# Performance work log

Hardware: AMD Instinct MI355X
Metric: run time of the kernel (lower is better)

Reference implementation:

```python
import jax, jax.numpy as jnp
import numpy as np

B, T, E, H = 4, 1024, 1024, 16
D = E // H  # head_size = 64
EPS = 1e-5


def layernorm(x, g, b):
    mu = jnp.mean(x, axis=-1, keepdims=True)
    var = jnp.mean(jnp.square(x - mu), axis=-1, keepdims=True)
    return (x - mu) * jax.lax.rsqrt(var + EPS) * g + b


def setup_inputs() -> dict:
    key = jax.random.key(0)
    ks = jax.random.split(key, 12)
    s = 0.02
    return {
        "x": jax.random.normal(ks[0], (B, T, E), dtype=jnp.float32),
        "ln1_g": jnp.ones((E,), jnp.float32),
        "ln1_b": jnp.zeros((E,), jnp.float32),
        "Wq": jax.random.normal(ks[1], (H, E, D), dtype=jnp.float32) * s,
        "Wk": jax.random.normal(ks[2], (H, E, D), dtype=jnp.float32) * s,
        "Wv": jax.random.normal(ks[3], (H, E, D), dtype=jnp.float32) * s,
        "Wp": jax.random.normal(ks[4], (E, E), dtype=jnp.float32) * s,
        "bp": jnp.zeros((E,), jnp.float32),
        "ln2_g": jnp.ones((E,), jnp.float32),
        "ln2_b": jnp.zeros((E,), jnp.float32),
        "W1": jax.random.normal(ks[5], (E, 4 * E), dtype=jnp.float32) * s,
        "b1": jnp.zeros((4 * E,), jnp.float32),
        "W2": jax.random.normal(ks[6], (4 * E, E), dtype=jnp.float32) * s,
        "b2": jnp.zeros((E,), jnp.float32),
    }


def reference(x, ln1_g, ln1_b, Wq, Wk, Wv, Wp, bp, ln2_g, ln2_b, W1, b1, W2, b2):
    # --- attention sub-block (pre-LN) ---
    h = layernorm(x, ln1_g, ln1_b)               # [B,T,E]
    q = jnp.einsum('bte,hed->bhtd', h, Wq)       # [B,H,T,D]
    k = jnp.einsum('bte,hed->bhtd', h, Wk)
    v = jnp.einsum('bte,hed->bhtd', h, Wv)
    # NOTE: original module has NO 1/sqrt(D) scaling and its 'tril' buffer is
    # all-ones, so masked_fill is a no-op -> full (non-causal) softmax.
    scores = jnp.einsum('bhtd,bhsd->bhts', q, k)  # [B,H,T,T]
    attn = jax.nn.softmax(scores, axis=-1)
    o = jnp.einsum('bhts,bhsd->bhtd', attn, v)    # [B,H,T,D]
    o = o.transpose(0, 2, 1, 3).reshape(x.shape[0], x.shape[1], -1)  # [B,T,E]
    x = x + o @ Wp + bp
    # --- feedforward sub-block (dropout is identity at eval) ---
    h2 = layernorm(x, ln2_g, ln2_b)
    x = x + jax.nn.relu(h2 @ W1 + b1) @ W2 + b2
    return x
```

## Files before the change

kernel.cpp:

```cpp
#include <hip/hip_runtime.h>
#include <hip/hip_bf16.h>

#define BB 4
#define TT 1024
#define EE 1024
#define HH 16
#define DD 64
#define MM 4096
#define NQKV 3072
#define E4 4096

using short8  = __attribute__((ext_vector_type(8))) short;
using short4v = __attribute__((ext_vector_type(4))) short;
using f32x4   = __attribute__((ext_vector_type(4))) float;

__device__ __forceinline__ short f2bf(float f) {
    __hip_bfloat16 h = __float2bfloat16(f);
    return *reinterpret_cast<short*>(&h);
}

__device__ __forceinline__ unsigned int cvtpk_bf16(float a, float b) {
    unsigned int w;
    asm("v_cvt_pk_bf16_f32 %0, %1, %2" : "=v"(w) : "v"(a), "v"(b));
    return w;
}

__device__ __forceinline__ void gld16(const void* g, void* l) {
    __builtin_amdgcn_global_load_lds((__attribute__((address_space(1))) void*)g,
                                     (__attribute__((address_space(3))) void*)l,
                                     16, 0, 0);
}

__global__ __launch_bounds__(256) void tcvt_kernel(const float* __restrict__ in,
                                                   short* __restrict__ out,
                                                   int R, int C) {
    __shared__ short tile[64][65];
    const int c0 = blockIdx.x * 64, r0 = blockIdx.y * 64;
    const int tr = threadIdx.x >> 6;
    const int tc = threadIdx.x & 63;
#pragma unroll
    for (int i = 0; i < 16; ++i) {
        int r = i * 4 + tr;
        tile[tc][r] = f2bf(in[(size_t)(r0 + r) * C + c0 + tc]);
    }
    __syncthreads();
#pragma unroll
    for (int i = 0; i < 16; ++i) {
        int c = i * 4 + tr;
        out[(size_t)(c0 + c) * R + r0 + tc] = tile[c][tc];
    }
}

__global__ __launch_bounds__(256) void pack_qkv_t(const float* __restrict__ Wq,
                                                  const float* __restrict__ Wk,
                                                  const float* __restrict__ Wv,
                                                  short* __restrict__ out) {
    __shared__ short tile[64][65];
    const int m = blockIdx.y;
    const int which = m >> 4, head = m & 15;
    const float* src = ((which == 0) ? Wq : (which == 1) ? Wk : Wv) + (size_t)head * EE * DD;
    const float scale = (which == 1) ? 1.44269504f : 1.0f;
    const int e0 = blockIdx.x * 64;
    const int tr = threadIdx.x >> 6, tc = threadIdx.x & 63;
#pragma unroll
    for (int i = 0; i < 16; ++i) {
        int e = i * 4 + tr;
        tile[tc][e] = f2bf(src[(size_t)(e0 + e) * DD + tc] * scale);
    }
    __syncthreads();
#pragma unroll
    for (int i = 0; i < 16; ++i) {
        int d = i * 4 + tr;
        out[(size_t)(which * 1024 + head * 64 + d) * EE + e0 + tc] = tile[d][tc];
    }
}

__global__ __launch_bounds__(256) void vtr_kernel(const short* __restrict__ qkv,
                                                  short* __restrict__ vT) {
    __shared__ short tile[64][68];
    const int b = blockIdx.z;
    const int t0 = blockIdx.x * 64, c0 = blockIdx.y * 64;
    const int tr = threadIdx.x >> 4;
    const int q4 = (threadIdx.x & 15) * 4;
#pragma unroll
    for (int i = 0; i < 4; ++i) {
        int t = i * 16 + tr;
        short4v v = *(const short4v*)&qkv[((size_t)b * TT + t0 + t) * NQKV + 2048 + c0 + q4];
        *(short4v*)&tile[t][q4] = v;
    }
    __syncthreads();
#pragma unroll
    for (int i = 0; i < 4; ++i) {
        int c = i * 16 + tr;
        short4v v;
        v[0] = tile[q4 + 0][c];
        v[1] = tile[q4 + 1][c];
        v[2] = tile[q4 + 2][c];
        v[3] = tile[q4 + 3][c];
        *(short4v*)&vT[((size_t)b * 1024 + c0 + c) * TT + t0 + q4] = v;
    }
}

__global__ __launch_bounds__(256) void ln_kernel(const float* __restrict__ x,
                                                 const float* __restrict__ g,
                                                 const float* __restrict__ b,
                                                 short* __restrict__ out) {
    __shared__ float red[4];
    const int row = blockIdx.x;
    const int tid = threadIdx.x;
    float4 v = *(const float4*)&x[(size_t)row * EE + tid * 4];
    float s = v.x + v.y + v.z + v.w;
#pragma unroll
    for (int off = 32; off >= 1; off >>= 1) s += __shfl_xor(s, off, 64);
    if ((tid & 63) == 0) red[tid >> 6] = s;
    __syncthreads();
    float mean = (red[0] + red[1] + red[2] + red[3]) * (1.0f / EE);
    __syncthreads();
    float d0 = v.x - mean, d1 = v.y - mean, d2 = v.z - mean, d3 = v.w - mean;
    s = d0 * d0 + d1 * d1 + d2 * d2 + d3 * d3;
#pragma unroll
    for (int off = 32; off >= 1; off >>= 1) s += __shfl_xor(s, off, 64);
    if ((tid & 63) == 0) red[tid >> 6] = s;
    __syncthreads();
    float var = (red[0] + red[1] + red[2] + red[3]) * (1.0f / EE);
    float rstd = rsqrtf(var + 1e-5f);
    int c = tid * 4;
    short4v o;
    o[0] = f2bf(d0 * rstd * g[c + 0] + b[c + 0]);
    o[1] = f2bf(d1 * rstd * g[c + 1] + b[c + 1]);
    o[2] = f2bf(d2 * rstd * g[c + 2] + b[c + 2]);
    o[3] = f2bf(d3 * rstd * g[c + 3] + b[c + 3]);
    *(short4v*)&out[(size_t)row * EE + c] = o;
}

template <bool HAS_BIAS, bool RELU>
__global__ __launch_bounds__(512, 2) void gemm256(const short* __restrict__ A,
                                                  const short* __restrict__ Bt,
                                                  const float* __restrict__ bias,
                                                  short* __restrict__ out,
                                                  int M, int N, int K) {
    __shared__ __align__(16) short Ab[2][2][8192];
    __shared__ __align__(16) short Bb[2][2][8192];

    const int tid = threadIdx.x;
    const int lane = tid & 63;
    const int wid = tid >> 6;
    const int wr = wid >> 2;
    const int wc = wid & 3;
    const int l15 = lane & 15, lhi = lane >> 4;
    const int rsw = l15 & 7;

    int wg = blockIdx.y * gridDim.x + blockIdx.x;
    const int chunk = (gridDim.x * gridDim.y) >> 3;
    wg = (wg & 7) * chunk + (wg >> 3);
    const int bx = wg % gridDim.x, by = wg / gridDim.x;
    const int row0 = by * 256, col0 = bx * 256;

    const int srow = tid >> 3;
    const int scol = (((tid & 7) ^ (srow & 7)) << 3);

    const int NT = K >> 6;

    f32x4 acc[8][4] = {};

    auto stageA = [&](int b, int h, int k0) {
#pragma unroll
        for (int j = 0; j < 2; ++j)
            gld16(&A[(size_t)(row0 + h * 128 + j * 64 + srow) * K + k0 + scol],
                  &Ab[b][h][j * 4096 + wid * 512]);
    };
    auto stageB = [&](int b, int h, int k0) {
#pragma unroll
        for (int j = 0; j < 2; ++j)
            gld16(&Bt[(size_t)(col0 + h * 128 + j * 64 + srow) * K + k0 + scol],
                  &Bb[b][h][j * 4096 + wid * 512]);
    };

    stageA(0, 0, 0); stageA(0, 1, 0);
    stageB(0, 0, 0); stageB(0, 1, 0);
    if (NT > 1) {
        stageB(1, 0, 64); stageB(1, 1, 64);
        asm volatile("s_waitcnt vmcnt(4)" ::: "memory");
    } else {
        asm volatile("s_waitcnt vmcnt(0)" ::: "memory");
    }
    __builtin_amdgcn_s_barrier();

    for (int u = 0; u < NT; ++u) {
        const int buf = u & 1;
        short8 bfr[4][2];
#pragma unroll
        for (int p = 0; p < 4; ++p) {
            if (p == 0) {
#pragma unroll
                for (int n = 0; n < 4; ++n)
#pragma unroll
                    for (int ks = 0; ks < 2; ++ks)
                        bfr[n][ks] = *(const short8*)&Bb[buf][wc >> 1]
                            [((wc & 1) * 64 + n * 16 + l15) * 64 +
                             (((ks << 2) + lhi) ^ rsw) * 8];
            }
            short8 af[2][2];
#pragma unroll
            for (int mi = 0; mi < 2; ++mi)
#pragma unroll
                for (int ks = 0; ks < 2; ++ks)
                    af[mi][ks] = *(const short8*)&Ab[buf][wr]
                        [((p * 2 + mi) * 16 + l15) * 64 +
                         (((ks << 2) + lhi) ^ rsw) * 8];
            if (p == 0 && u + 1 < NT) stageA(buf ^ 1, 0, (u + 1) << 6);
            if (p == 1 && u + 1 < NT) stageA(buf ^ 1, 1, (u + 1) << 6);
            if (p == 2 && u + 2 < NT) stageB(buf, 0, (u + 2) << 6);
            if (p == 3 && u + 2 < NT) stageB(buf, 1, (u + 2) << 6);
            __builtin_amdgcn_s_barrier();
            __builtin_amdgcn_s_setprio(1);
#pragma unroll
            for (int mi = 0; mi < 2; ++mi)
#pragma unroll
                for (int n = 0; n < 4; ++n)
#pragma unroll
                    for (int ks = 0; ks < 2; ++ks)
                        acc[p * 2 + mi][n] = __builtin_amdgcn_mfma_f32_16x16x32_bf16(
                            af[mi][ks], bfr[n][ks], acc[p * 2 + mi][n], 0, 0, 0);
            __builtin_amdgcn_s_setprio(0);
            if (p == 3 && u + 1 < NT) {
                if (u + 2 < NT) asm volatile("s_waitcnt vmcnt(4)" ::: "memory");
                else            asm volatile("s_waitcnt vmcnt(0)" ::: "memory");
            }
            __builtin_amdgcn_s_barrier();
        }
    }

#pragma unroll
    for (int m = 0; m < 8; ++m)
#pragma unroll
        for (int n = 0; n < 4; ++n)
#pragma unroll
            for (int r = 0; r < 4; ++r) {
                int row = row0 + wr * 128 + m * 16 + lhi * 4 + r;
                int col = col0 + wc * 64 + n * 16 + l15;
                float v = acc[m][n][r];
                if (HAS_BIAS) v += bias[col];
                if (RELU) v = fmaxf(v, 0.f);
                out[(size_t)row * N + col] = f2bf(v);
            }
}

template <int BN, int PIPE, bool HAS_BIAS, bool RELU, bool RESID, bool OUT_BF16>
__global__ __launch_bounds__(256) void gemm_bt(const short* __restrict__ A,
                                               const short* __restrict__ Bt,
                                               const float* __restrict__ bias,
                                               const float* __restrict__ resid,
                                               void* __restrict__ outp,
                                               int M, int N, int K) {
    constexpr int WRC = (BN == 128) ? 2 : 4;
    constexpr int WCC = (BN == 128) ? 2 : 1;
    constexpr int MI = 8 / WRC;
    constexpr int NI = BN / (16 * WCC);
    constexpr int BCH = BN / 32;
    constexpr int ASZ = 128 * 64, BSZ = BN * 64;

    __shared__ __align__(16) short As[(PIPE ? 2 : 1) * ASZ];
    __shared__ __align__(16) short Bs[(PIPE ? 2 : 1) * BSZ];

    const int tid = threadIdx.x;
    const int lane = tid & 63;
    const int wid = tid >> 6;
    const int wr = (WRC == 2) ? (wid >> 1) : wid;
    const int wc = (WCC == 2) ? (wid & 1) : 0;
    const int l15 = lane & 15, lhi = lane >> 4;

    int wg = blockIdx.y * gridDim.x + blockIdx.x;
    const int chunk = (gridDim.x * gridDim.y) >> 3;
    wg = (wg & 7) * chunk + (wg >> 3);
    const int bx = wg % gridDim.x;
    const int by = wg / gridDim.x;
    const int row0 = by * 128, col0 = bx * BN;

    const int srow = tid >> 3;
    const int scol = (((tid & 7) ^ (srow & 7)) << 3);
    const int rsw = l15 & 7;

    const int wrow0 = wr * (16 * MI);
    const int wcol0 = wc * (16 * NI);

    f32x4 acc[MI][NI] = {};

    auto stage = [&](int k0, int bs) {
#pragma unroll
        for (int ch = 0; ch < 4; ++ch)
            gld16(&A[(size_t)(row0 + ch * 32 + srow) * K + k0 + scol],
                  &As[bs * ASZ + ch * 2048 + wid * 512]);
#pragma unroll
        for (int ch = 0; ch < BCH; ++ch)
            gld16(&Bt[(size_t)(col0 + ch * 32 + srow) * K + k0 + scol],
                  &Bs[bs * BSZ + ch * 2048 + wid * 512]);
    };
    auto compute = [&](int bs) {
#pragma unroll
        for (int ks = 0; ks < 2; ++ks) {
            short8 af[MI], bf[NI];
#pragma unroll
            for (int mi = 0; mi < MI; ++mi)
                af[mi] = *(const short8*)&As[bs * ASZ + (wrow0 + mi * 16 + l15) * 64 +
                                             (((ks << 2) + lhi) ^ rsw) * 8];
#pragma unroll
            for (int ni = 0; ni < NI; ++ni)
                bf[ni] = *(const short8*)&Bs[bs * BSZ + (wcol0 + ni * 16 + l15) * 64 +
                                             (((ks << 2) + lhi) ^ rsw) * 8];
#pragma unroll
            for (int mi = 0; mi < MI; ++mi)
#pragma unroll
                for (int ni = 0; ni < NI; ++ni)
                    acc[mi][ni] = __builtin_amdgcn_mfma_f32_16x16x32_bf16(
                        af[mi], bf[ni], acc[mi][ni], 0, 0, 0);
        }
    };

    if (PIPE == 1) {
        const int nt = K >> 6;
        stage(0, 0);
        stage(64, 1);
        int cur = 0;
        for (int t = 0; t < nt; ++t) {
            if (t + 1 < nt) asm volatile("s_waitcnt vmcnt(6)" ::: "memory");
            else            asm volatile("s_waitcnt vmcnt(0)" ::: "memory");
            __builtin_amdgcn_s_barrier();
            __builtin_amdgcn_sched_barrier(0);
            compute(cur);
            __builtin_amdgcn_sched_barrier(0);
            __builtin_amdgcn_s_barrier();
            if (t + 2 < nt) stage((t + 2) << 6, cur);
            cur ^= 1;
        }
    } else {
        for (int k0 = 0; k0 < K; k0 += 64) {
            __syncthreads();
            stage(k0, 0);
            __syncthreads();
            compute(0);
        }
    }

    float* outf = (float*)outp;
    short* outb = (short*)outp;
#pragma unroll
    for (int mi = 0; mi < MI; ++mi)
#pragma unroll
        for (int ni = 0; ni < NI; ++ni)
#pragma unroll
            for (int r = 0; r < 4; ++r) {
                int row = row0 + wrow0 + mi * 16 + lhi * 4 + r;
                int col = col0 + wcol0 + ni * 16 + l15;
                float v = acc[mi][ni][r];
                if (HAS_BIAS) v += bias[col];
                if (RELU) v = fmaxf(v, 0.f);
                if (RESID) v += resid[(size_t)row * N + col];
                if (OUT_BF16) outb[(size_t)row * N + col] = f2bf(v);
                else outf[(size_t)row * N + col] = v;
            }
}

__global__ __launch_bounds__(256) void attn_kernel(const short* __restrict__ qkv,
                                                   const short* __restrict__ vT,
                                                   short* __restrict__ obuf) {
    __shared__ __align__(16) short Ks[2][64 * 64];
    __shared__ __align__(16) short Vs[2][64 * 64];
    __shared__ __align__(16) unsigned int Pl[4][2][16][40];
    const int tid = threadIdx.x;
    const int lane = tid & 63;
    const int wid = tid >> 6;
    const int l15 = lane & 15, lhi = lane >> 4;
    const int lhi4 = lhi * 4;

    const int nb = ((blockIdx.x & 7) << 6) + (blockIdx.x >> 3);
    const int b = nb >> 7;
    const int h = (nb >> 3) & 15;
    const int q0 = (nb & 7) << 7;
    const size_t rbase = (size_t)b * TT;
    const int hq = h * 64;
    const short* vg = vT + ((size_t)b * 1024 + hq) * TT;

    const int srow = tid >> 3;
    const int scol = (((tid & 7) ^ (srow & 7)) << 3);
    const int rsw = (l15 & 7);

    short8 aq[2][2];
#pragma unroll
    for (int g = 0; g < 2; ++g)
#pragma unroll
        for (int ks = 0; ks < 2; ++ks)
            aq[g][ks] = *(const short8*)&qkv[(rbase + q0 + wid * 32 + g * 16 + l15) * NQKV +
                                             hq + ks * 32 + lhi * 8];

    float mrun[2] = {-INFINITY, -INFINITY};
    float lsum[2] = {0.f, 0.f};
    f32x4 o[2][4] = {};

#pragma unroll
    for (int ch = 0; ch < 2; ++ch) {
        gld16(&qkv[(rbase + 0 + ch * 32 + srow) * NQKV + 1024 + hq + scol],
              &Ks[0][ch * 2048 + wid * 512]);
        gld16(&vg[(size_t)(ch * 32 + srow) * TT + 0 + scol],
              &Vs[0][ch * 2048 + wid * 512]);
    }
    __syncthreads();

    int cur = 0;
    for (int st = 0; st < TT; st += 64) {
        if (st + 64 < TT) {
#pragma unroll
            for (int ch = 0; ch < 2; ++ch) {
                gld16(&qkv[(rbase + st + 64 + ch * 32 + srow) * NQKV + 1024 + hq + scol],
                      &Ks[cur ^ 1][ch * 2048 + wid * 512]);
                gld16(&vg[(size_t)(ch * 32 + srow) * TT + st + 64 + scol],
                      &Vs[cur ^ 1][ch * 2048 + wid * 512]);
            }
        }
        const short* K = &Ks[cur][0];
        const short* V = &Vs[cur][0];

        short8 kf[4][2];
#pragma unroll
        for (int nt = 0; nt < 4; ++nt)
#pragma unroll
            for (int ks = 0; ks < 2; ++ks)
                kf[nt][ks] = *(const short8*)&K[(nt * 16 + l15) * 64 +
                                               (((ks << 2) + lhi) ^ rsw) * 8];

        short8 pa[2][2];
#pragma unroll
        for (int g = 0; g < 2; ++g) {
            f32x4 stv[4] = {};
#pragma unroll
            for (int nt = 0; nt < 4; ++nt)
#pragma unroll
                for (int ks = 0; ks < 2; ++ks)
                    stv[nt] = __builtin_amdgcn_mfma_f32_16x16x32_bf16(
                        kf[nt][ks], aq[g][ks], stv[nt], 0, 0, 0);
            float tn[4];
#pragma unroll
            for (int nt = 0; nt < 4; ++nt)
                tn[nt] = fmaxf(fmaxf(stv[nt][0], stv[nt][1]),
                               fmaxf(stv[nt][2], stv[nt][3]));
            float tm = fmaxf(fmaxf(tn[0], tn[1]), fmaxf(tn[2], tn[3]));
            tm = fmaxf(tm, __shfl_xor(tm, 16, 64));
            tm = fmaxf(tm, __shfl_xor(tm, 32, 64));
            const bool full = !__all(tm - mrun[g] <= 11.5f);
            if (full) {
                float mnew = fmaxf(mrun[g], tm);
                float fac = exp2f(mrun[g] - mnew);
                mrun[g] = mnew;
                lsum[g] *= fac;
                float f0 = __shfl(fac, lhi4 + 0, 64);
                float f1 = __shfl(fac, lhi4 + 1, 64);
                float f2 = __shfl(fac, lhi4 + 2, 64);
                float f3 = __shfl(fac, lhi4 + 3, 64);
#pragma unroll
                for (int dt = 0; dt < 4; ++dt) {
                    o[g][dt][0] *= f0; o[g][dt][1] *= f1;
                    o[g][dt][2] *= f2; o[g][dt][3] *= f3;
                }
            }
            float pv[4][4];
            float sn[4];
#pragma unroll
            for (int nt = 0; nt < 4; ++nt) {
#pragma unroll
                for (int r = 0; r < 4; ++r) pv[nt][r] = exp2f(stv[nt][r] - mrun[g]);
                sn[nt] = (pv[nt][0] + pv[nt][1]) + (pv[nt][2] + pv[nt][3]);
            }
            float rs = (sn[0] + sn[1]) + (sn[2] + sn[3]);
            rs += __shfl_xor(rs, 16, 64);
            rs += __shfl_xor(rs, 32, 64);
            lsum[g] += rs;
#pragma unroll
            for (int nt = 0; nt < 4; ++nt) {
                uint2 ww;
                ww.x = cvtpk_bf16(pv[nt][0], pv[nt][1]);
                ww.y = cvtpk_bf16(pv[nt][2], pv[nt][3]);
                *(uint2*)&Pl[wid][g][l15][nt * 8 + lhi * 2] = ww;
            }
            pa[g][0] = *(const short8*)&Pl[wid][g][l15][lhi4];
            pa[g][1] = *(const short8*)&Pl[wid][g][l15][16 + lhi4];
        }

        short8 vf[4][2];
#pragma unroll
        for (int dt = 0; dt < 4; ++dt)
#pragma unroll
            for (int k2 = 0; k2 < 2; ++k2)
                vf[dt][k2] = *(const short8*)&V[(dt * 16 + l15) * 64 +
                                               (((k2 << 2) + lhi) ^ rsw) * 8];
#pragma unroll
        for (int g = 0; g < 2; ++g)
#pragma unroll
            for (int dt = 0; dt < 4; ++dt)
#pragma unroll
                for (int k2 = 0; k2 < 2; ++k2)
                    o[g][dt] = __builtin_amdgcn_mfma_f32_16x16x32_bf16(
                        pa[g][k2], vf[dt][k2], o[g][dt], 0, 0, 0);

        __syncthreads();
        cur ^= 1;
    }
#pragma unroll
    for (int g = 0; g < 2; ++g) {
        float inv = 1.0f / lsum[g];
        float i0 = __shfl(inv, lhi4 + 0, 64);
        float i1 = __shfl(inv, lhi4 + 1, 64);
        float i2 = __shfl(inv, lhi4 + 2, 64);
        float i3 = __shfl(inv, lhi4 + 3, 64);
#pragma unroll
        for (int dt = 0; dt < 4; ++dt) {
            int col = hq + dt * 16 + l15;
            size_t rw = rbase + q0 + wid * 32 + g * 16 + lhi4;
            obuf[(rw + 0) * EE + col] = f2bf(o[g][dt][0] * i0);
            obuf[(rw + 1) * EE + col] = f2bf(o[g][dt][1] * i1);
            obuf[(rw + 2) * EE + col] = f2bf(o[g][dt][2] * i2);
            obuf[(rw + 3) * EE + col] = f2bf(o[g][dt][3] * i3);
        }
    }
}

extern "C" void kernel_launch(void* const* d_in, const int* in_sizes, int n_in,
                              void* d_out, int out_size, void* d_ws, size_t ws_size,
                              hipStream_t stream) {
    const float* x   = (const float*)d_in[0];
    const float* g1  = (const float*)d_in[1];
    const float* be1 = (const float*)d_in[2];
    const float* Wq  = (const float*)d_in[3];
    const float* Wk  = (const float*)d_in[4];
    const float* Wv  = (const float*)d_in[5];
    const float* Wp  = (const float*)d_in[6];
    const float* bp  = (const float*)d_in[7];
    const float* g2  = (const float*)d_in[8];
    const float* be2 = (const float*)d_in[9];
    const float* W1  = (const float*)d_in[10];
    const float* b1f = (const float*)d_in[11];
    const float* W2  = (const float*)d_in[12];
    const float* b2f = (const float*)d_in[13];

    char* p = (char*)d_ws;
    short* h_bf   = (short*)p; p += (size_t)MM * EE * 2;
    short* wqkv   = (short*)p; p += (size_t)EE * NQKV * 2;
    short* qkv    = (short*)p; p += (size_t)MM * NQKV * 2;
    short* o_bf   = (short*)p; p += (size_t)MM * EE * 2;
    short* wp_bf  = (short*)p; p += (size_t)EE * EE * 2;
    float* x1     = (float*)p; p += (size_t)MM * EE * 4;
    short* h2_bf  = (short*)p; p += (size_t)MM * EE * 2;
    short* w1_bf  = (short*)p; p += (size_t)EE * E4 * 2;
    short* mid_bf = (short*)p; p += (size_t)MM * E4 * 2;
    short* w2_bf  = (short*)p; p += (size_t)E4 * EE * 2;
    short* vTb    = (short*)p; p += (size_t)BB * 1024 * TT * 2;

    pack_qkv_t<<<dim3(16, 48), 256, 0, stream>>>(Wq, Wk, Wv, wqkv);
    tcvt_kernel<<<dim3(16, 16), 256, 0, stream>>>(Wp, wp_bf, EE, EE);
    tcvt_kernel<<<dim3(64, 16), 256, 0, stream>>>(W1, w1_bf, EE, E4);
    tcvt_kernel<<<dim3(16, 64), 256, 0, stream>>>(W2, w2_bf, E4, EE);

    ln_kernel<<<MM, 256, 0, stream>>>(x, g1, be1, h_bf);

    gemm256<false, false>
        <<<dim3(NQKV / 256, MM / 256), 512, 0, stream>>>(h_bf, wqkv, nullptr,
                                                         qkv, MM, NQKV, EE);

    vtr_kernel<<<dim3(16, 16, BB), 256, 0, stream>>>(qkv, vTb);

    attn_kernel<<<BB * HH * (TT / 128), 256, 0, stream>>>(qkv, vTb, o_bf);

    gemm_bt<64, 1, true, false, true, false>
        <<<dim3(EE / 64, MM / 128), 256, 0, stream>>>(o_bf, wp_bf, bp, x, x1, MM, EE, EE);

    ln_kernel<<<MM, 256, 0, stream>>>(x1, g2, be2, h2_bf);

    gemm256<true, true>
        <<<dim3(E4 / 256, MM / 256), 512, 0, stream>>>(h2_bf, w1_bf, b1f,
                                                       mid_bf, MM, E4, EE);

    gemm_bt<64, 1, true, false, true, false>
        <<<dim3(EE / 64, MM / 128), 256, 0, stream>>>(mid_bf, w2_bf, b2f, x1,
                                                      (float*)d_out, MM, EE, E4);
}
```

Baseline: 221.3 us.

## Split-K the W2 projection GEMM and deepen the gemm_bt pipeline to three stages

```diff
diff --git a/kernel.cpp b/kernel.cpp
--- a/kernel.cpp
+++ b/kernel.cpp
@@ -133,6 +133,24 @@
     *(short4v*)&out[(size_t)row * EE + c] = o;
 }
 
+__global__ __launch_bounds__(256) void redk_kernel(const float* __restrict__ p0,
+                                                   const float* __restrict__ p1,
+                                                   const float* __restrict__ bias,
+                                                   const float* __restrict__ resid,
+                                                   float* __restrict__ out) {
+    const int i = (blockIdx.x * 256 + threadIdx.x) * 4;
+    float4 a = *(const float4*)&p0[i];
+    float4 b = *(const float4*)&p1[i];
+    float4 r = *(const float4*)&resid[i];
+    float4 c = *(const float4*)&bias[i & 1023];
+    float4 o;
+    o.x = a.x + b.x + r.x + c.x;
+    o.y = a.y + b.y + r.y + c.y;
+    o.z = a.z + b.z + r.z + c.z;
+    o.w = a.w + b.w + r.w + c.w;
+    *(float4*)&out[i] = o;
+}
+
 template <bool HAS_BIAS, bool RELU>
 __global__ __launch_bounds__(512, 2) void gemm256(const short* __restrict__ A,
                                                   const short* __restrict__ Bt,
@@ -246,7 +264,7 @@
             }
 }
 
-template <int BN, int PIPE, bool HAS_BIAS, bool RELU, bool RESID, bool OUT_BF16>
+template <int BN, int PIPE, int SPLIT, bool HAS_BIAS, bool RELU, bool RESID, bool OUT_BF16>
 __global__ __launch_bounds__(256) void gemm_bt(const short* __restrict__ A,
                                                const short* __restrict__ Bt,
                                                const float* __restrict__ bias,
@@ -259,9 +277,10 @@
     constexpr int NI = BN / (16 * WCC);
     constexpr int BCH = BN / 32;
     constexpr int ASZ = 128 * 64, BSZ = BN * 64;
-
-    __shared__ __align__(16) short As[(PIPE ? 2 : 1) * ASZ];
-    __shared__ __align__(16) short Bs[(PIPE ? 2 : 1) * BSZ];
+    constexpr int NBUF = PIPE ? 3 : 1;
+
+    __shared__ __align__(16) short As[NBUF * ASZ];
+    __shared__ __align__(16) short Bs[NBUF * BSZ];
 
     const int tid = threadIdx.x;
     const int lane = tid & 63;
@@ -277,6 +296,9 @@
     const int by = wg / gridDim.x;
     const int row0 = by * 128, col0 = bx * BN;
 
+    const int Keff = SPLIT ? (K >> 1) : K;
+    const int kb = SPLIT ? blockIdx.z * Keff : 0;
+
     const int srow = tid >> 3;
     const int scol = (((tid & 7) ^ (srow & 7)) << 3);
     const int rsw = l15 & 7;
@@ -318,20 +340,23 @@
     };
 
     if (PIPE == 1) {
-        const int nt = K >> 6;
-        stage(0, 0);
-        stage(64, 1);
+        const int nt = Keff >> 6;
+        stage(kb, 0);
+        stage(kb + 64, 1);
+        stage(kb + 128, 2);
         int cur = 0;
         for (int t = 0; t < nt; ++t) {
-            if (t + 1 < nt) asm volatile("s_waitcnt vmcnt(6)" ::: "memory");
-            else            asm volatile("s_waitcnt vmcnt(0)" ::: "memory");
+            const int rem = nt - 1 - t;
+            if (rem >= 2)      asm volatile("s_waitcnt vmcnt(12)" ::: "memory");
+            else if (rem == 1) asm volatile("s_waitcnt vmcnt(6)" ::: "memory");
+            else               asm volatile("s_waitcnt vmcnt(0)" ::: "memory");
             __builtin_amdgcn_s_barrier();
             __builtin_amdgcn_sched_barrier(0);
             compute(cur);
             __builtin_amdgcn_sched_barrier(0);
             __builtin_amdgcn_s_barrier();
-            if (t + 2 < nt) stage((t + 2) << 6, cur);
-            cur ^= 1;
+            if (t + 3 < nt) stage(kb + ((t + 3) << 6), cur);
+            cur = (cur == 2) ? 0 : cur + 1;
         }
     } else {
         for (int k0 = 0; k0 < K; k0 += 64) {
@@ -344,6 +369,7 @@
 
     float* outf = (float*)outp;
     short* outb = (short*)outp;
+    if (SPLIT) outf += (size_t)blockIdx.z * M * N;
 #pragma unroll
     for (int mi = 0; mi < MI; ++mi)
 #pragma unroll
@@ -353,9 +379,11 @@
                 int row = row0 + wrow0 + mi * 16 + lhi * 4 + r;
                 int col = col0 + wcol0 + ni * 16 + l15;
                 float v = acc[mi][ni][r];
-                if (HAS_BIAS) v += bias[col];
-                if (RELU) v = fmaxf(v, 0.f);
-                if (RESID) v += resid[(size_t)row * N + col];
+                if (!SPLIT) {
+                    if (HAS_BIAS) v += bias[col];
+                    if (RELU) v = fmaxf(v, 0.f);
+                    if (RESID) v += resid[(size_t)row * N + col];
+                }
                 if (OUT_BF16) outb[(size_t)row * N + col] = f2bf(v);
                 else outf[(size_t)row * N + col] = v;
             }
@@ -554,6 +582,8 @@
     short* w2_bf  = (short*)p; p += (size_t)E4 * EE * 2;
     short* vTb    = (short*)p; p += (size_t)BB * 1024 * TT * 2;
 
+    float* part = (float*)qkv;
+
     pack_qkv_t<<<dim3(16, 48), 256, 0, stream>>>(Wq, Wk, Wv, wqkv);
     tcvt_kernel<<<dim3(16, 16), 256, 0, stream>>>(Wp, wp_bf, EE, EE);
     tcvt_kernel<<<dim3(64, 16), 256, 0, stream>>>(W1, w1_bf, EE, E4);
@@ -569,7 +599,7 @@
 
     attn_kernel<<<BB * HH * (TT / 128), 256, 0, stream>>>(qkv, vTb, o_bf);
 
-    gemm_bt<64, 1, true, false, true, false>
+    gemm_bt<64, 1, 0, true, false, true, false>
         <<<dim3(EE / 64, MM / 128), 256, 0, stream>>>(o_bf, wp_bf, bp, x, x1, MM, EE, EE);
 
     ln_kernel<<<MM, 256, 0, stream>>>(x1, g2, be2, h2_bf);
@@ -578,7 +608,9 @@
         <<<dim3(E4 / 256, MM / 256), 512, 0, stream>>>(h2_bf, w1_bf, b1f,
                                                        mid_bf, MM, E4, EE);
 
-    gemm_bt<64, 1, true, false, true, false>
-        <<<dim3(EE / 64, MM / 128), 256, 0, stream>>>(mid_bf, w2_bf, b2f, x1,
-                                                      (float*)d_out, MM, EE, E4);
-}
+    gemm_bt<64, 1, 1, false, false, false, false>
+        <<<dim3(EE / 64, MM / 128, 2), 256, 0, stream>>>(mid_bf, w2_bf, nullptr, nullptr,
+                                                         part, MM, EE, E4);
+    redk_kernel<<<(MM * EE / 4) / 256, 256, 0, stream>>>(part, part + (size_t)MM * EE,
+                                                         b2f, x1, (float*)d_out);
+}
```

Measured after the change: 231.2 us. 1.04x slower.

## Halve attention query tile per block to double grid size, add MFMA priority hints

Applied to the files above, without the earlier changes.

```diff
diff --git a/kernel.cpp b/kernel.cpp
--- a/kernel.cpp
+++ b/kernel.cpp
@@ -366,17 +366,17 @@
                                                    short* __restrict__ obuf) {
     __shared__ __align__(16) short Ks[2][64 * 64];
     __shared__ __align__(16) short Vs[2][64 * 64];
-    __shared__ __align__(16) unsigned int Pl[4][2][16][40];
+    __shared__ __align__(16) unsigned int Pl[4][16][40];
     const int tid = threadIdx.x;
     const int lane = tid & 63;
     const int wid = tid >> 6;
     const int l15 = lane & 15, lhi = lane >> 4;
     const int lhi4 = lhi * 4;
 
-    const int nb = ((blockIdx.x & 7) << 6) + (blockIdx.x >> 3);
-    const int b = nb >> 7;
-    const int h = (nb >> 3) & 15;
-    const int q0 = (nb & 7) << 7;
+    const int nb = ((blockIdx.x & 7) << 7) + (blockIdx.x >> 3);
+    const int b = nb >> 8;
+    const int h = (nb >> 4) & 15;
+    const int q0 = (nb & 15) << 6;
     const size_t rbase = (size_t)b * TT;
     const int hq = h * 64;
     const short* vg = vT + ((size_t)b * 1024 + hq) * TT;
@@ -385,17 +385,14 @@
     const int scol = (((tid & 7) ^ (srow & 7)) << 3);
     const int rsw = (l15 & 7);
 
-    short8 aq[2][2];
-#pragma unroll
-    for (int g = 0; g < 2; ++g)
-#pragma unroll
-        for (int ks = 0; ks < 2; ++ks)
-            aq[g][ks] = *(const short8*)&qkv[(rbase + q0 + wid * 32 + g * 16 + l15) * NQKV +
-                                             hq + ks * 32 + lhi * 8];
-
-    float mrun[2] = {-INFINITY, -INFINITY};
-    float lsum[2] = {0.f, 0.f};
-    f32x4 o[2][4] = {};
+    short8 aq[2];
+#pragma unroll
+    for (int ks = 0; ks < 2; ++ks)
+        aq[ks] = *(const short8*)&qkv[(rbase + q0 + wid * 16 + l15) * NQKV +
+                                      hq + ks * 32 + lhi * 8];
+
+    float mrun = -INFINITY, lsum = 0.f;
+    f32x4 o[4] = {};
 
 #pragma unroll
     for (int ch = 0; ch < 2; ++ch) {
@@ -420,106 +417,93 @@
         const short* K = &Ks[cur][0];
         const short* V = &Vs[cur][0];
 
-        short8 kf[4][2];
+        f32x4 stv[4] = {};
+        __builtin_amdgcn_s_setprio(1);
 #pragma unroll
         for (int nt = 0; nt < 4; ++nt)
 #pragma unroll
-            for (int ks = 0; ks < 2; ++ks)
-                kf[nt][ks] = *(const short8*)&K[(nt * 16 + l15) * 64 +
+            for (int ks = 0; ks < 2; ++ks) {
+                short8 kf = *(const short8*)&K[(nt * 16 + l15) * 64 +
                                                (((ks << 2) + lhi) ^ rsw) * 8];
-
-        short8 pa[2][2];
-#pragma unroll
-        for (int g = 0; g < 2; ++g) {
-            f32x4 stv[4] = {};
-#pragma unroll
-            for (int nt = 0; nt < 4; ++nt)
-#pragma unroll
-                for (int ks = 0; ks < 2; ++ks)
-                    stv[nt] = __builtin_amdgcn_mfma_f32_16x16x32_bf16(
-                        kf[nt][ks], aq[g][ks], stv[nt], 0, 0, 0);
-            float tn[4];
-#pragma unroll
-            for (int nt = 0; nt < 4; ++nt)
-                tn[nt] = fmaxf(fmaxf(stv[nt][0], stv[nt][1]),
-                               fmaxf(stv[nt][2], stv[nt][3]));
-            float tm = fmaxf(fmaxf(tn[0], tn[1]), fmaxf(tn[2], tn[3]));
-            tm = fmaxf(tm, __shfl_xor(tm, 16, 64));
-            tm = fmaxf(tm, __shfl_xor(tm, 32, 64));
-            const bool full = !__all(tm - mrun[g] <= 11.5f);
-            if (full) {
-                float mnew = fmaxf(mrun[g], tm);
-                float fac = exp2f(mrun[g] - mnew);
-                mrun[g] = mnew;
-                lsum[g] *= fac;
-                float f0 = __shfl(fac, lhi4 + 0, 64);
-                float f1 = __shfl(fac, lhi4 + 1, 64);
-                float f2 = __shfl(fac, lhi4 + 2, 64);
-                float f3 = __shfl(fac, lhi4 + 3, 64);
-#pragma unroll
-                for (int dt = 0; dt < 4; ++dt) {
-                    o[g][dt][0] *= f0; o[g][dt][1] *= f1;
-                    o[g][dt][2] *= f2; o[g][dt][3] *= f3;
-                }
-            }
-            float pv[4][4];
-            float sn[4];
-#pragma unroll
-            for (int nt = 0; nt < 4; ++nt) {
-#pragma unroll
-                for (int r = 0; r < 4; ++r) pv[nt][r] = exp2f(stv[nt][r] - mrun[g]);
-                sn[nt] = (pv[nt][0] + pv[nt][1]) + (pv[nt][2] + pv[nt][3]);
-            }
-            float rs = (sn[0] + sn[1]) + (sn[2] + sn[3]);
-            rs += __shfl_xor(rs, 16, 64);
-            rs += __shfl_xor(rs, 32, 64);
-            lsum[g] += rs;
-#pragma unroll
-            for (int nt = 0; nt < 4; ++nt) {
-                uint2 ww;
-                ww.x = cvtpk_bf16(pv[nt][0], pv[nt][1]);
-                ww.y = cvtpk_bf16(pv[nt][2], pv[nt][3]);
-                *(uint2*)&Pl[wid][g][l15][nt * 8 + lhi * 2] = ww;
-            }
-            pa[g][0] = *(const short8*)&Pl[wid][g][l15][lhi4];
-            pa[g][1] = *(const short8*)&Pl[wid][g][l15][16 + lhi4];
-        }
-
-        short8 vf[4][2];
+                stv[nt] = __builtin_amdgcn_mfma_f32_16x16x32_bf16(kf, aq[ks],
+                                                                  stv[nt], 0, 0, 0);
+            }
+        __builtin_amdgcn_s_setprio(0);
+
+        float tn[4];
+#pragma unroll
+        for (int nt = 0; nt < 4; ++nt)
+            tn[nt] = fmaxf(fmaxf(stv[nt][0], stv[nt][1]),
+                           fmaxf(stv[nt][2], stv[nt][3]));
+        float tm = fmaxf(fmaxf(tn[0], tn[1]), fmaxf(tn[2], tn[3]));
+        tm = fmaxf(tm, __shfl_xor(tm, 16, 64));
+        tm = fmaxf(tm, __shfl_xor(tm, 32, 64));
+        const bool full = !__all(tm - mrun <= 11.5f);
+        if (full) {
+            float mnew = fmaxf(mrun, tm);
+            float fac = exp2f(mrun - mnew);
+            mrun = mnew;
+            lsum *= fac;
+            float f0 = __shfl(fac, lhi4 + 0, 64);
+            float f1 = __shfl(fac, lhi4 + 1, 64);
+            float f2 = __shfl(fac, lhi4 + 2, 64);
+            float f3 = __shfl(fac, lhi4 + 3, 64);
+#pragma unroll
+            for (int dt = 0; dt < 4; ++dt) {
+                o[dt][0] *= f0; o[dt][1] *= f1;
+                o[dt][2] *= f2; o[dt][3] *= f3;
+            }
+        }
+        float pv[4][4], sn[4];
+#pragma unroll
+        for (int nt = 0; nt < 4; ++nt) {
+#pragma unroll
+            for (int r = 0; r < 4; ++r) pv[nt][r] = exp2f(stv[nt][r] - mrun);
+            sn[nt] = (pv[nt][0] + pv[nt][1]) + (pv[nt][2] + pv[nt][3]);
+        }
+        float rs = (sn[0] + sn[1]) + (sn[2] + sn[3]);
+        rs += __shfl_xor(rs, 16, 64);
+        rs += __shfl_xor(rs, 32, 64);
+        lsum += rs;
+#pragma unroll
+        for (int nt = 0; nt < 4; ++nt) {
+            uint2 ww;
+            ww.x = cvtpk_bf16(pv[nt][0], pv[nt][1]);
+            ww.y = cvtpk_bf16(pv[nt][2], pv[nt][3]);
+            *(uint2*)&Pl[wid][l15][nt * 8 + lhi * 2] = ww;
+        }
+        short8 pa[2];
+        pa[0] = *(const short8*)&Pl[wid][l15][lhi4];
+        pa[1] = *(const short8*)&Pl[wid][l15][16 + lhi4];
+
+        __builtin_amdgcn_s_setprio(1);
 #pragma unroll
         for (int dt = 0; dt < 4; ++dt)
 #pragma unroll
-            for (int k2 = 0; k2 < 2; ++k2)
-                vf[dt][k2] = *(const short8*)&V[(dt * 16 + l15) * 64 +
+            for (int k2 = 0; k2 < 2; ++k2) {
+                short8 vf = *(const short8*)&V[(dt * 16 + l15) * 64 +
                                                (((k2 << 2) + lhi) ^ rsw) * 8];
-#pragma unroll
-        for (int g = 0; g < 2; ++g)
-#pragma unroll
-            for (int dt = 0; dt < 4; ++dt)
-#pragma unroll
-                for (int k2 = 0; k2 < 2; ++k2)
-                    o[g][dt] = __builtin_amdgcn_mfma_f32_16x16x32_bf16(
-                        pa[g][k2], vf[dt][k2], o[g][dt], 0, 0, 0);
+                o[dt] = __builtin_amdgcn_mfma_f32_16x16x32_bf16(pa[k2], vf,
+                                                                o[dt], 0, 0, 0);
+            }
+        __builtin_amdgcn_s_setprio(0);
 
         __syncthreads();
         cur ^= 1;
     }
-#pragma unroll
-    for (int g = 0; g < 2; ++g) {
-        float inv = 1.0f / lsum[g];
-        float i0 = __shfl(inv, lhi4 + 0, 64);
-        float i1 = __shfl(inv, lhi4 + 1, 64);
-        float i2 = __shfl(inv, lhi4 + 2, 64);
-        float i3 = __shfl(inv, lhi4 + 3, 64);
-#pragma unroll
-        for (int dt = 0; dt < 4; ++dt) {
-            int col = hq + dt * 16 + l15;
-            size_t rw = rbase + q0 + wid * 32 + g * 16 + lhi4;
-            obuf[(rw + 0) * EE + col] = f2bf(o[g][dt][0] * i0);
-            obuf[(rw + 1) * EE + col] = f2bf(o[g][dt][1] * i1);
-            obuf[(rw + 2) * EE + col] = f2bf(o[g][dt][2] * i2);
-            obuf[(rw + 3) * EE + col] = f2bf(o[g][dt][3] * i3);
-        }
+    float inv = 1.0f / lsum;
+    float i0 = __shfl(inv, lhi4 + 0, 64);
+    float i1 = __shfl(inv, lhi4 + 1, 64);
+    float i2 = __shfl(inv, lhi4 + 2, 64);
+    float i3 = __shfl(inv, lhi4 + 3, 64);
+#pragma unroll
+    for (int dt = 0; dt < 4; ++dt) {
+        int col = hq + dt * 16 + l15;
+        size_t rw = rbase + q0 + wid * 16 + lhi4;
+        obuf[(rw + 0) * EE + col] = f2bf(o[dt][0] * i0);
+        obuf[(rw + 1) * EE + col] = f2bf(o[dt][1] * i1);
+        obuf[(rw + 2) * EE + col] = f2bf(o[dt][2] * i2);
+        obuf[(rw + 3) * EE + col] = f2bf(o[dt][3] * i3);
     }
 }
 
@@ -567,7 +551,7 @@
 
     vtr_kernel<<<dim3(16, 16, BB), 256, 0, stream>>>(qkv, vTb);
 
-    attn_kernel<<<BB * HH * (TT / 128), 256, 0, stream>>>(qkv, vTb, o_bf);
+    attn_kernel<<<BB * HH * (TT / 64), 256, 0, stream>>>(qkv, vTb, o_bf);
 
     gemm_bt<64, 1, true, false, true, false>
         <<<dim3(EE / 64, MM / 128), 256, 0, stream>>>(o_bf, wp_bf, bp, x, x1, MM, EE, EE);
```

Measured after the change: 229.0 us. +3.5%, slower.

## Split-K the W2 GEMM onto 256x256 tile kernel with reduction pass

Applied to the files above, without the earlier changes.

```diff
diff --git a/kernel.cpp b/kernel.cpp
--- a/kernel.cpp
+++ b/kernel.cpp
@@ -133,12 +133,33 @@
     *(short4v*)&out[(size_t)row * EE + c] = o;
 }
 
-template <bool HAS_BIAS, bool RELU>
+__global__ __launch_bounds__(256) void redk4_kernel(const float* __restrict__ p012,
+                                                    const float* __restrict__ p3,
+                                                    const float* __restrict__ bias,
+                                                    const float* __restrict__ resid,
+                                                    float* __restrict__ out) {
+    const size_t i = ((size_t)blockIdx.x * 256 + threadIdx.x) * 4;
+    float4 a = *(const float4*)&p012[i];
+    float4 b = *(const float4*)&p012[i + (size_t)MM * EE];
+    float4 c = *(const float4*)&p012[i + (size_t)2 * MM * EE];
+    float4 d = *(const float4*)&p3[i];
+    float4 r = *(const float4*)&resid[i];
+    float4 bb = *(const float4*)&bias[i & 1023];
+    float4 o;
+    o.x = (a.x + b.x) + (c.x + d.x) + r.x + bb.x;
+    o.y = (a.y + b.y) + (c.y + d.y) + r.y + bb.y;
+    o.z = (a.z + b.z) + (c.z + d.z) + r.z + bb.z;
+    o.w = (a.w + b.w) + (c.w + d.w) + r.w + bb.w;
+    *(float4*)&out[i] = o;
+}
+
+template <bool HAS_BIAS, bool RELU, bool SPLIT>
 __global__ __launch_bounds__(512, 2) void gemm256(const short* __restrict__ A,
                                                   const short* __restrict__ Bt,
                                                   const float* __restrict__ bias,
-                                                  short* __restrict__ out,
-                                                  int M, int N, int K) {
+                                                  void* __restrict__ outp,
+                                                  void* __restrict__ outp3,
+                                                  int M, int N, int K, int lda) {
     __shared__ __align__(16) short Ab[2][2][8192];
     __shared__ __align__(16) short Bb[2][2][8192];
 
@@ -156,6 +177,8 @@
     const int bx = wg % gridDim.x, by = wg / gridDim.x;
     const int row0 = by * 256, col0 = bx * 256;
 
+    const int kb = SPLIT ? blockIdx.z * K : 0;
+
     const int srow = tid >> 3;
     const int scol = (((tid & 7) ^ (srow & 7)) << 3);
 
@@ -166,13 +189,13 @@
     auto stageA = [&](int b, int h, int k0) {
 #pragma unroll
         for (int j = 0; j < 2; ++j)
-            gld16(&A[(size_t)(row0 + h * 128 + j * 64 + srow) * K + k0 + scol],
+            gld16(&A[(size_t)(row0 + h * 128 + j * 64 + srow) * lda + kb + k0 + scol],
                   &Ab[b][h][j * 4096 + wid * 512]);
     };
     auto stageB = [&](int b, int h, int k0) {
 #pragma unroll
         for (int j = 0; j < 2; ++j)
-            gld16(&Bt[(size_t)(col0 + h * 128 + j * 64 + srow) * K + k0 + scol],
+            gld16(&Bt[(size_t)(col0 + h * 128 + j * 64 + srow) * lda + kb + k0 + scol],
                   &Bb[b][h][j * 4096 + wid * 512]);
     };
 
@@ -231,6 +254,11 @@
         }
     }
 
+    short* outb = (short*)outp;
+    float* outf = nullptr;
+    if (SPLIT)
+        outf = (blockIdx.z == 3) ? (float*)outp3
+                                 : (float*)outp + (size_t)blockIdx.z * M * N;
 #pragma unroll
     for (int m = 0; m < 8; ++m)
 #pragma unroll
@@ -240,9 +268,13 @@
                 int row = row0 + wr * 128 + m * 16 + lhi * 4 + r;
                 int col = col0 + wc * 64 + n * 16 + l15;
                 float v = acc[m][n][r];
-                if (HAS_BIAS) v += bias[col];
-                if (RELU) v = fmaxf(v, 0.f);
-                out[(size_t)row * N + col] = f2bf(v);
+                if (SPLIT) {
+                    outf[(size_t)row * N + col] = v;
+                } else {
+                    if (HAS_BIAS) v += bias[col];
+                    if (RELU) v = fmaxf(v, 0.f);
+                    outb[(size_t)row * N + col] = f2bf(v);
+                }
             }
 }
 
@@ -432,12 +464,14 @@
 #pragma unroll
         for (int g = 0; g < 2; ++g) {
             f32x4 stv[4] = {};
+            __builtin_amdgcn_s_setprio(1);
 #pragma unroll
             for (int nt = 0; nt < 4; ++nt)
 #pragma unroll
                 for (int ks = 0; ks < 2; ++ks)
                     stv[nt] = __builtin_amdgcn_mfma_f32_16x16x32_bf16(
                         kf[nt][ks], aq[g][ks], stv[nt], 0, 0, 0);
+            __builtin_amdgcn_s_setprio(0);
             float tn[4];
 #pragma unroll
             for (int nt = 0; nt < 4; ++nt)
@@ -492,6 +526,7 @@
             for (int k2 = 0; k2 < 2; ++k2)
                 vf[dt][k2] = *(const short8*)&V[(dt * 16 + l15) * 64 +
                                                (((k2 << 2) + lhi) ^ rsw) * 8];
+        __builtin_amdgcn_s_setprio(1);
 #pragma unroll
         for (int g = 0; g < 2; ++g)
 #pragma unroll
@@ -500,6 +535,7 @@
                 for (int k2 = 0; k2 < 2; ++k2)
                     o[g][dt] = __builtin_amdgcn_mfma_f32_16x16x32_bf16(
                         pa[g][k2], vf[dt][k2], o[g][dt], 0, 0, 0);
+        __builtin_amdgcn_s_setprio(0);
 
         __syncthreads();
         cur ^= 1;
@@ -554,6 +590,9 @@
     short* w2_bf  = (short*)p; p += (size_t)E4 * EE * 2;
     short* vTb    = (short*)p; p += (size_t)BB * 1024 * TT * 2;
 
+    float* part012 = (float*)d_ws;
+    float* part3   = (float*)h2_bf;
+
     pack_qkv_t<<<dim3(16, 48), 256, 0, stream>>>(Wq, Wk, Wv, wqkv);
     tcvt_kernel<<<dim3(16, 16), 256, 0, stream>>>(Wp, wp_bf, EE, EE);
     tcvt_kernel<<<dim3(64, 16), 256, 0, stream>>>(W1, w1_bf, EE, E4);
@@ -561,9 +600,9 @@
 
     ln_kernel<<<MM, 256, 0, stream>>>(x, g1, be1, h_bf);
 
-    gemm256<false, false>
+    gemm256<false, false, false>
         <<<dim3(NQKV / 256, MM / 256), 512, 0, stream>>>(h_bf, wqkv, nullptr,
-                                                         qkv, MM, NQKV, EE);
+                                                         qkv, nullptr, MM, NQKV, EE, EE);
 
     vtr_kernel<<<dim3(16, 16, BB), 256, 0, stream>>>(qkv, vTb);
 
@@ -574,11 +613,14 @@
 
     ln_kernel<<<MM, 256, 0, stream>>>(x1, g2, be2, h2_bf);
 
-    gemm256<true, true>
+    gemm256<true, true, false>
         <<<dim3(E4 / 256, MM / 256), 512, 0, stream>>>(h2_bf, w1_bf, b1f,
-                                                       mid_bf, MM, E4, EE);
-
-    gemm_bt<64, 1, true, false, true, false>
-        <<<dim3(EE / 64, MM / 128), 256, 0, stream>>>(mid_bf, w2_bf, b2f, x1,
-                                                      (float*)d_out, MM, EE, E4);
-}
+                                                       mid_bf, nullptr, MM, E4, EE, EE);
+
+    gemm256<false, false, true>
+        <<<dim3(EE / 256, MM / 256, 4), 512, 0, stream>>>(mid_bf, w2_bf, nullptr,
+                                                          part012, part3,
+                                                          MM, EE, 1024, E4);
+    redk4_kernel<<<(MM * EE / 4) / 256, 256, 0, stream>>>(part012, part3, b2f, x1,
+                                                          (float*)d_out);
+}
```

New measurement: 225.5 us. About the same (+1.9%).
